# Performance work log

Hardware: AMD Instinct MI355X
Metric: run time of the kernel (lower is better)

Reference implementation:

```python
import jax, jax.numpy as jnp
import numpy as np

DIM = 768
HEADS = 12
HD = DIM // HEADS
B, NX, NY = 8, 1024, 1024
GRID = 32
FREQ = 100.0
MLP_HID = 4 * DIM
EPS = 1e-5


def _grid_pos(batch, n, grid):
    g = int(np.sqrt(n))
    yy, xx = jnp.meshgrid(jnp.arange(g, dtype=jnp.int32), jnp.arange(g, dtype=jnp.int32), indexing='ij')
    pos = jnp.stack([yy.reshape(-1), xx.reshape(-1)], axis=-1)  # [N,2]
    return jnp.broadcast_to(pos[None], (batch, n, 2))


def setup_inputs() -> dict:
    key = jax.random.key(0)
    ks = jax.random.split(key, 16)
    s = 0.02
    inp = {
        'x': jax.random.normal(ks[0], (B, NX, DIM), jnp.float32),
        'y': jax.random.normal(ks[1], (B, NY, DIM), jnp.float32),
        'xpos': _grid_pos(B, NX, GRID),
        'ypos': _grid_pos(B, NY, GRID),
        # norms (gamma, beta)
        'norm1_g': jnp.ones((DIM,), jnp.float32), 'norm1_b': jnp.zeros((DIM,), jnp.float32),
        'norm2_g': jnp.ones((DIM,), jnp.float32), 'norm2_b': jnp.zeros((DIM,), jnp.float32),
        'norm3_g': jnp.ones((DIM,), jnp.float32), 'norm3_b': jnp.zeros((DIM,), jnp.float32),
        'normy_g': jnp.ones((DIM,), jnp.float32), 'normy_b': jnp.zeros((DIM,), jnp.float32),
        # self-attn: fused qkv (no bias, qkv_bias=False), out proj (with bias)
        'qkv_w': jax.random.normal(ks[2], (DIM, 3 * DIM), jnp.float32) * s,
        'attn_proj_w': jax.random.normal(ks[3], (DIM, DIM), jnp.float32) * s,
        'attn_proj_b': jnp.zeros((DIM,), jnp.float32),
        # cross-attn: separate q/k/v (no bias), out proj (with bias)
        'projq_w': jax.random.normal(ks[4], (DIM, DIM), jnp.float32) * s,
        'projk_w': jax.random.normal(ks[5], (DIM, DIM), jnp.float32) * s,
        'projv_w': jax.random.normal(ks[6], (DIM, DIM), jnp.float32) * s,
        'cross_proj_w': jax.random.normal(ks[7], (DIM, DIM), jnp.float32) * s,
        'cross_proj_b': jnp.zeros((DIM,), jnp.float32),
        # MLP
        'fc1_w': jax.random.normal(ks[8], (DIM, MLP_HID), jnp.float32) * s,
        'fc1_b': jnp.zeros((MLP_HID,), jnp.float32),
        'fc2_w': jax.random.normal(ks[9], (MLP_HID, DIM), jnp.float32) * s,
        'fc2_b': jnp.zeros((DIM,), jnp.float32),
    }
    return inp


def layernorm(x, g, b):
    m = jnp.mean(x, axis=-1, keepdims=True)
    v = jnp.mean(jnp.square(x - m), axis=-1, keepdims=True)
    return (x - m) * jax.lax.rsqrt(v + EPS) * g + b


def rope1d(tok, pos):
    # tok: [B,H,N,D], pos: [B,N] int
    D = tok.shape[-1]
    inv = 1.0 / (FREQ ** (jnp.arange(0, D, 2, dtype=jnp.float32) / D))  # [D/2]
    f = pos[:, None, :, None].astype(jnp.float32) * inv  # [B,1,N,D/2]
    emb = jnp.concatenate([f, f], axis=-1)  # [B,1,N,D]
    cos, sin = jnp.cos(emb), jnp.sin(emb)
    t1, t2 = jnp.split(tok, 2, axis=-1)
    rot = jnp.concatenate([-t2, t1], axis=-1)
    return tok * cos + rot * sin


def rope2d(tok, pos):
    # first half of head dim rotated by y-coord, second half by x-coord
    ty, tx = jnp.split(tok, 2, axis=-1)
    return jnp.concatenate([rope1d(ty, pos[..., 0]), rope1d(tx, pos[..., 1])], axis=-1)


def sdpa(q, k, v):
    scale = q.shape[-1] ** -0.5
    a = jax.nn.softmax(jnp.einsum('bhqd,bhkd->bhqk', q, k) * scale, axis=-1)
    return jnp.einsum('bhqk,bhkd->bhqd', a, v)


def split_heads(t):  # [B,N,C] -> [B,H,N,HD]
    Bv, N, C = t.shape
    return t.reshape(Bv, N, HEADS, HD).transpose(0, 2, 1, 3)


def merge_heads(t):  # [B,H,N,HD] -> [B,N,C]
    Bv, H, N, D = t.shape
    return t.transpose(0, 2, 1, 3).reshape(Bv, N, H * D)


def reference(x, y, xpos, ypos,
              norm1_g, norm1_b, norm2_g, norm2_b, norm3_g, norm3_b, normy_g, normy_b,
              qkv_w, attn_proj_w, attn_proj_b,
              projq_w, projk_w, projv_w, cross_proj_w, cross_proj_b,
              fc1_w, fc1_b, fc2_w, fc2_b):
    # --- self attention ---
    h = layernorm(x, norm1_g, norm1_b)
    qkv = h @ qkv_w  # [B,N,3C]
    q, k, v = (split_heads(t) for t in jnp.split(qkv, 3, axis=-1))
    q = rope2d(q, xpos)
    k = rope2d(k, xpos)
    x = x + merge_heads(sdpa(q, k, v)) @ attn_proj_w + attn_proj_b

    # --- cross attention ---
    y_ = layernorm(y, normy_g, normy_b)
    hq = layernorm(x, norm2_g, norm2_b)
    q = rope2d(split_heads(hq @ projq_w), xpos)
    k = rope2d(split_heads(y_ @ projk_w), ypos)
    v = split_heads(y_ @ projv_w)
    x = x + merge_heads(sdpa(q, k, v)) @ cross_proj_w + cross_proj_b

    # --- MLP ---
    h = layernorm(x, norm3_g, norm3_b)
    x = x + jax.nn.gelu(h @ fc1_w + fc1_b, approximate=False) @ fc2_w + fc2_b
    return (x, y)
```

## Files before the change

kernel.cpp:

```cpp
#include <hip/hip_runtime.h>
#include <hip/hip_bf16.h>
#include <math.h>

#define DIM 768
#define HEADS 12
#define HD 64
#define BB 8
#define NN 1024
#define EPSV 1e-5f

typedef unsigned int uint32;
typedef unsigned short ushort_t;
using short8 = __attribute__((ext_vector_type(8))) short;
using f32x4 = __attribute__((ext_vector_type(4))) float;

static __device__ inline ushort_t f2b(float v) {
    uint32 u = __float_as_uint(v);
    return (ushort_t)((u + 0x7FFFu + ((u >> 16) & 1u)) >> 16);
}
static __device__ inline float b2f(ushort_t v) {
    return __uint_as_float((uint32)v << 16);
}

static __device__ inline float erf_fast(float x) {
    float ax = fabsf(x);
    float t = __frcp_rn(1.0f + 0.3275911f * ax);
    float p = t * (0.254829592f + t * (-0.284496736f + t * (1.421413741f +
              t * (-1.453152027f + t * 1.061405429f))));
    float e = 1.0f - p * __expf(-ax * ax);
    return copysignf(e, x);
}

static __device__ __forceinline__ void gload_lds16(const ushort_t* g, ushort_t* l) {
    __builtin_amdgcn_global_load_lds(
        (const __attribute__((address_space(1))) void*)g,
        (__attribute__((address_space(3))) void*)l, 16, 0, 0);
}

__global__ __launch_bounds__(256) void ln_bf16(const float* __restrict__ in,
                                               const float* __restrict__ g,
                                               const float* __restrict__ b,
                                               ushort_t* __restrict__ out) {
    int r = blockIdx.x;
    const float* x = in + (size_t)r * DIM;
    ushort_t* o = out + (size_t)r * DIM;
    int t = threadIdx.x;
    float v0 = x[t], v1 = x[t + 256], v2 = x[t + 512];
    float s = v0 + v1 + v2;
    float s2 = v0 * v0 + v1 * v1 + v2 * v2;
    for (int off = 32; off; off >>= 1) {
        s += __shfl_xor(s, off);
        s2 += __shfl_xor(s2, off);
    }
    __shared__ float ls[4], lq[4];
    int wid = t >> 6;
    if ((t & 63) == 0) { ls[wid] = s; lq[wid] = s2; }
    __syncthreads();
    s = ls[0] + ls[1] + ls[2] + ls[3];
    s2 = lq[0] + lq[1] + lq[2] + lq[3];
    float mean = s * (1.0f / DIM);
    float var = s2 * (1.0f / DIM) - mean * mean;
    float rs = rsqrtf(var + EPSV);
    o[t]       = f2b((v0 - mean) * rs * g[t]       + b[t]);
    o[t + 256] = f2b((v1 - mean) * rs * g[t + 256] + b[t + 256]);
    o[t + 512] = f2b((v2 - mean) * rs * g[t + 512] + b[t + 512]);
}

struct XArgs {
    const float* src[8];
    ushort_t* dst[8];
    int K[8], N[8];
    int tstart[9];
};
__global__ __launch_bounds__(256) void xform_w(XArgs a) {
    __shared__ float tl[32][33];
    int t = blockIdx.x;
    int w = 0;
    while (t >= a.tstart[w + 1]) w++;
    int lt = t - a.tstart[w];
    int ntn = a.N[w] >> 5;
    int k0 = (lt / ntn) * 32, n0 = (lt % ntn) * 32;
    const float* src = a.src[w];
    ushort_t* dst = a.dst[w];
    int K = a.K[w], N = a.N[w];
    int rr = threadIdx.x >> 5, cc = threadIdx.x & 31;
#pragma unroll
    for (int u = 0; u < 4; u++)
        tl[rr + u * 8][cc] = src[(size_t)(k0 + rr + u * 8) * N + n0 + cc];
    __syncthreads();
#pragma unroll
    for (int u = 0; u < 4; u++)
        dst[(size_t)(n0 + rr + u * 8) * K + k0 + cc] = f2b(tl[cc][rr + u * 8]);
}

template <int ACT, int OBF16>
__global__ __launch_bounds__(256) void gemm_mfma(const ushort_t* __restrict__ A,
                                                 const ushort_t* __restrict__ Wt,
                                                 const float* __restrict__ bias,
                                                 const float* res,
                                                 void* Cout, int M, int N, int K) {
    __shared__ ushort_t lds[4][128 * 32];
    int bid = blockIdx.x;
    int xcd = bid & 7, rr = bid >> 3;
    int bx = rr >> 3;
    int by = xcd * 8 + (rr & 7);
    int m0 = by * 128, n0 = bx * 128;
    int tid = threadIdx.x;
    int wid = tid >> 6, lane = tid & 63;
    int wm = wid >> 1, wn = wid & 1;
    int l15 = lane & 15, lh = lane >> 4;

    int srow = lane >> 2, cslot = lane & 3;

    auto STAGE = [&](int buf, int k0) {
#pragma unroll
        for (int inst = 0; inst < 2; inst++) {
            int r0 = (wid * 2 + inst) * 16 + srow;
            int swzr = (r0 & 3) ^ ((r0 >> 2) & 3);
            int csrc = (cslot ^ swzr) << 3;
            gload_lds16(A + (size_t)(m0 + r0) * K + k0 + csrc,
                        &lds[buf * 2 + 0][(wid * 2 + inst) * 512]);
            gload_lds16(Wt + (size_t)(n0 + r0) * K + k0 + csrc,
                        &lds[buf * 2 + 1][(wid * 2 + inst) * 512]);
        }
    };

    STAGE(0, 0);
    f32x4 acc[4][4] = {};
    __syncthreads();

    int nT = K >> 5;
    int cur = 0;
    for (int t = 0; t < nT; t++) {
        if (t + 1 < nT) STAGE(cur ^ 1, (t + 1) << 5);
        short8 af[4], bfr[4];
#pragma unroll
        for (int i = 0; i < 4; i++) {
            int rA = wm * 64 + i * 16 + l15;
            int sA = lh ^ ((rA & 3) ^ ((rA >> 2) & 3));
            af[i] = *(const short8*)&lds[cur * 2 + 0][rA * 32 + (sA << 3)];
            int rB = wn * 64 + i * 16 + l15;
            int sB = lh ^ ((rB & 3) ^ ((rB >> 2) & 3));
            bfr[i] = *(const short8*)&lds[cur * 2 + 1][rB * 32 + (sB << 3)];
        }
#pragma unroll
        for (int i = 0; i < 4; i++)
#pragma unroll
            for (int j = 0; j < 4; j++)
                acc[i][j] = __builtin_amdgcn_mfma_f32_16x16x32_bf16(
                    af[i], bfr[j], acc[i][j], 0, 0, 0);
        __syncthreads();
        cur ^= 1;
    }

    float* ep = (float*)&lds[0][0] + wid * 1088;
    int erow = lane >> 2, ecol = (lane & 3) * 16;
#pragma unroll
    for (int i = 0; i < 4; i++) {
#pragma unroll
        for (int j = 0; j < 4; j++) {
            int n = n0 + wn * 64 + j * 16 + l15;
            float bv = bias ? bias[n] : 0.0f;
#pragma unroll
            for (int r = 0; r < 4; r++) {
                float v = acc[i][j][r] + bv;
                if (ACT == 1) v = 0.5f * v * (1.0f + erf_fast(v * 0.70710678118654752f));
                ep[(lh * 4 + r) * 68 + j * 16 + l15] = v;
            }
        }
        int m = m0 + wm * 64 + i * 16 + erow;
        size_t off = (size_t)m * N + n0 + wn * 64 + ecol;
        float vv[16];
#pragma unroll
        for (int u = 0; u < 4; u++)
            *(float4*)&vv[u * 4] = *(float4*)&ep[erow * 68 + ecol + u * 4];
        if (res) {
#pragma unroll
            for (int u = 0; u < 4; u++) {
                float4 rv = *(const float4*)(res + off + u * 4);
                vv[u * 4 + 0] += rv.x;
                vv[u * 4 + 1] += rv.y;
                vv[u * 4 + 2] += rv.z;
                vv[u * 4 + 3] += rv.w;
            }
        }
        if (OBF16) {
            ushort_t tb[16];
#pragma unroll
            for (int u = 0; u < 16; u++) tb[u] = f2b(vv[u]);
            *(uint4*)((ushort_t*)Cout + off)     = *(uint4*)&tb[0];
            *(uint4*)((ushort_t*)Cout + off + 8) = *(uint4*)&tb[8];
        } else {
#pragma unroll
            for (int u = 0; u < 4; u++)
                *(float4*)((float*)Cout + off + u * 4) = *(float4*)&vv[u * 4];
        }
    }
}

__global__ __launch_bounds__(256) void rope2_bf16(ushort_t* __restrict__ ta,
                                                  const int* __restrict__ pa, int sa,
                                                  ushort_t* __restrict__ tb,
                                                  const int* __restrict__ pb, int sb,
                                                  int rt) {
    int idx = blockIdx.x * 256 + threadIdx.x;
    ushort_t* t;
    const int* pos;
    int rowStride;
    if (idx >= rt) { idx -= rt; t = tb; pos = pb; rowStride = sb; }
    else           { t = ta; pos = pa; rowStride = sa; }
    int i = idx & 15;
    int half = (idx >> 4) & 1;
    int h = (idx >> 5) % HEADS;
    int bn = idx / (HEADS * 32);
    int p = pos[(size_t)bn * 2 + half];
    float inv = powf(100.0f, -(float)i / 16.0f);
    float f = (float)p * inv;
    float c, s;
    sincosf(f, &s, &c);
    ushort_t* base = t + (size_t)bn * rowStride + h * HD + half * 32;
    float t1 = b2f(base[i]), t2 = b2f(base[i + 16]);
    base[i]      = f2b(t1 * c - t2 * s);
    base[i + 16] = f2b(t2 * c + t1 * s);
}

__global__ __launch_bounds__(256) void transpose_v(const ushort_t* __restrict__ src,
                                                   int ss, ushort_t* __restrict__ dst) {
    __shared__ ushort_t tl[64][66];
    int bid = blockIdx.x;
    int nt = bid & 15;
    int h = (bid >> 4) % HEADS;
    int b = bid / (16 * HEADS);
    int n0 = nt * 64;
    int t = threadIdx.x;
    int r = t >> 2, c0 = (t & 3) * 16;
    const ushort_t* s = src + ((size_t)(b * NN) + n0 + r) * ss + h * HD + c0;
    *(uint4*)&tl[r][c0]     = *(const uint4*)s;
    *(uint4*)&tl[r][c0 + 8] = *(const uint4*)(s + 8);
    __syncthreads();
    ushort_t* d = dst + (((size_t)(b * HEADS + h)) * HD + r) * NN + n0 + c0;
    ushort_t tmp[16];
#pragma unroll
    for (int u = 0; u < 16; u++) tmp[u] = tl[c0 + u][r];
    *(uint4*)d       = *(uint4*)tmp;
    *(uint4*)(d + 8) = *(uint4*)(tmp + 8);
}

__global__ __launch_bounds__(256) void attn_mfma(const ushort_t* __restrict__ Q, int sq,
                                                 const ushort_t* __restrict__ K, int sk,
                                                 const ushort_t* __restrict__ VT,
                                                 ushort_t* __restrict__ O, int so) {
    __shared__ ushort_t Qs[64][72];
    __shared__ ushort_t Ks[64][72];
    __shared__ ushort_t Vs[64][72];
    __shared__ ushort_t Ps[64][72];

    int g = blockIdx.x;
    int bid = (g & 7) * 192 + (g >> 3);
    int qb = bid & 15;
    int h = (bid >> 4) % HEADS;
    int b = bid / (16 * HEADS);
    int n0 = qb * 64;

    int tid = threadIdx.x;
    int lane = tid & 63, wq = tid >> 6;
    int l15 = lane & 15, lh = lane >> 4;

    const ushort_t* Qbase = Q + (size_t)b * NN * sq + h * HD;
    const ushort_t* Kbase = K + (size_t)b * NN * sk + h * HD;
    const ushort_t* VTbase = VT + ((size_t)(b * HEADS + h)) * HD * NN;
    ushort_t* Obase = O + (size_t)b * NN * so + h * HD;

    int row = tid >> 2, c0 = (tid & 3) * 16;
    {
        const ushort_t* src = Qbase + (size_t)(n0 + row) * sq + c0;
        uint4 q0 = *(const uint4*)src;
        uint4 q1 = *(const uint4*)(src + 8);
        ushort_t* qp0 = (ushort_t*)&q0;
        ushort_t* qp1 = (ushort_t*)&q1;
        ushort_t t0[8], t1[8];
#pragma unroll
        for (int u = 0; u < 8; u++) {
            t0[u] = f2b(b2f(qp0[u]) * 0.125f);
            t1[u] = f2b(b2f(qp1[u]) * 0.125f);
        }
        *(uint4*)&Qs[row][c0]     = *(uint4*)t0;
        *(uint4*)&Qs[row][c0 + 8] = *(uint4*)t1;
    }

    const ushort_t* kp = Kbase + (size_t)row * sk + c0;
    const ushort_t* vp = VTbase + (size_t)row * NN + c0;
    uint4 rk0 = *(const uint4*)kp, rk1 = *(const uint4*)(kp + 8);
    uint4 rv0 = *(const uint4*)vp, rv1 = *(const uint4*)(vp + 8);

    short8 ones;
#pragma unroll
    for (int u = 0; u < 8; u++) ones[u] = (short)0x3F80;

    f32x4 oacc[4] = {};
    f32x4 oaccS = {};
    float mrow[4] = {-1e30f, -1e30f, -1e30f, -1e30f};

    for (int kt = 0; kt < NN / 64; kt++) {
        __syncthreads();
        *(uint4*)&Ks[row][c0]     = rk0;
        *(uint4*)&Ks[row][c0 + 8] = rk1;
        *(uint4*)&Vs[row][c0]     = rv0;
        *(uint4*)&Vs[row][c0 + 8] = rv1;
        __syncthreads();
        if (kt + 1 < NN / 64) {
            const ushort_t* kp2 = kp + (size_t)(kt + 1) * 64 * sk;
            const ushort_t* vp2 = vp + (size_t)(kt + 1) * 64;
            rk0 = *(const uint4*)kp2;
            rk1 = *(const uint4*)(kp2 + 8);
            rv0 = *(const uint4*)vp2;
            rv1 = *(const uint4*)(vp2 + 8);
        }

        f32x4 s[4] = {};
#pragma unroll
        for (int ks8 = 0; ks8 < 2; ks8++) {
            short8 aq = *(const short8*)&Qs[wq * 16 + l15][ks8 * 32 + lh * 8];
#pragma unroll
            for (int j = 0; j < 4; j++) {
                short8 bk = *(const short8*)&Ks[j * 16 + l15][ks8 * 32 + lh * 8];
                s[j] = __builtin_amdgcn_mfma_f32_16x16x32_bf16(aq, bk, s[j], 0, 0, 0);
            }
        }

        float corr[4];
#pragma unroll
        for (int r = 0; r < 4; r++) {
            float v0 = s[0][r], v1 = s[1][r], v2 = s[2][r], v3 = s[3][r];
            float rm = fmaxf(fmaxf(v0, v1), fmaxf(v2, v3));
            rm = fmaxf(rm, __shfl_xor(rm, 1));
            rm = fmaxf(rm, __shfl_xor(rm, 2));
            rm = fmaxf(rm, __shfl_xor(rm, 4));
            rm = fmaxf(rm, __shfl_xor(rm, 8));
            float mn = fmaxf(mrow[r], rm);
            corr[r] = __expf(mrow[r] - mn);
            mrow[r] = mn;
            float p0 = __expf(v0 - mn), p1 = __expf(v1 - mn);
            float p2 = __expf(v2 - mn), p3 = __expf(v3 - mn);
            int qrow = wq * 16 + lh * 4 + r;
            Ps[qrow][0 * 16 + l15] = f2b(p0);
            Ps[qrow][1 * 16 + l15] = f2b(p1);
            Ps[qrow][2 * 16 + l15] = f2b(p2);
            Ps[qrow][3 * 16 + l15] = f2b(p3);
        }
#pragma unroll
        for (int r = 0; r < 4; r++) {
            oaccS[r] *= corr[r];
#pragma unroll
            for (int j = 0; j < 4; j++) oacc[j][r] *= corr[r];
        }

#pragma unroll
        for (int ks8 = 0; ks8 < 2; ks8++) {
            short8 ap = *(const short8*)&Ps[wq * 16 + l15][ks8 * 32 + lh * 8];
#pragma unroll
            for (int j = 0; j < 4; j++) {
                short8 bv = *(const short8*)&Vs[j * 16 + l15][ks8 * 32 + lh * 8];
                oacc[j] = __builtin_amdgcn_mfma_f32_16x16x32_bf16(ap, bv, oacc[j], 0, 0, 0);
            }
            oaccS = __builtin_amdgcn_mfma_f32_16x16x32_bf16(ap, ones, oaccS, 0, 0, 0);
        }
    }

#pragma unroll
    for (int r = 0; r < 4; r++) {
        float inv = 1.0f / oaccS[r];
        int prow = wq * 16 + lh * 4 + r;
#pragma unroll
        for (int j = 0; j < 4; j++)
            Ps[prow][j * 16 + l15] = f2b(oacc[j][r] * inv);
    }
    int erow = lane >> 2, ecol = (lane & 3) * 16;
    uint4 w0 = *(uint4*)&Ps[wq * 16 + erow][ecol];
    uint4 w1 = *(uint4*)&Ps[wq * 16 + erow][ecol + 8];
    ushort_t* op = Obase + (size_t)(n0 + wq * 16 + erow) * so + ecol;
    *(uint4*)op       = w0;
    *(uint4*)(op + 8) = w1;
}

__global__ __launch_bounds__(256) void fill_f32(float* __restrict__ out, float v, int n) {
    int i = blockIdx.x * 256 + threadIdx.x;
    if (i < n) out[i] = v;
}

extern "C" void kernel_launch(void* const* d_in, const int* in_sizes, int n_in,
                              void* d_out, int out_size, void* d_ws, size_t ws_size,
                              hipStream_t stream) {
    const float* x = (const float*)d_in[0];
    const float* y = (const float*)d_in[1];
    const int* xpos = (const int*)d_in[2];
    const int* ypos = (const int*)d_in[3];
    const float* norm1_g = (const float*)d_in[4];
    const float* norm1_b = (const float*)d_in[5];
    const float* norm2_g = (const float*)d_in[6];
    const float* norm2_b = (const float*)d_in[7];
    const float* norm3_g = (const float*)d_in[8];
    const float* norm3_b = (const float*)d_in[9];
    const float* normy_g = (const float*)d_in[10];
    const float* normy_b = (const float*)d_in[11];
    const float* qkv_w = (const float*)d_in[12];
    const float* attn_proj_w = (const float*)d_in[13];
    const float* attn_proj_b = (const float*)d_in[14];
    const float* projq_w = (const float*)d_in[15];
    const float* projk_w = (const float*)d_in[16];
    const float* projv_w = (const float*)d_in[17];
    const float* cross_proj_w = (const float*)d_in[18];
    const float* cross_proj_b = (const float*)d_in[19];
    const float* fc1_w = (const float*)d_in[20];
    const float* fc1_b = (const float*)d_in[21];
    const float* fc2_w = (const float*)d_in[22];
    const float* fc2_b = (const float*)d_in[23];
    float* out = (float*)d_out;

    const size_t SZ = (size_t)BB * NN * DIM;
    const int ROWS = BB * NN;

    const size_t WS_NEED = SZ * 4 + SZ * 2 + 4 * SZ * 2 + 9437184ull * 2;

    {
        const int expect[24] = {
            (int)SZ, (int)SZ, BB * NN * 2, BB * NN * 2,
            DIM, DIM, DIM, DIM, DIM, DIM, DIM, DIM,
            DIM * 3 * DIM, DIM * DIM, DIM,
            DIM * DIM, DIM * DIM, DIM * DIM, DIM * DIM, DIM,
            DIM * 4 * DIM, 4 * DIM, 4 * DIM * DIM, DIM};
        float sentinel = 0.0f;
        if (n_in != 24) sentinel = 2000.0f;
        else {
            for (int i = 0; i < 24; i++)
                if (in_sizes[i] != expect[i]) { sentinel = 1000.0f + i; break; }
        }
        if (sentinel == 0.0f && ws_size < WS_NEED) sentinel = 3000.0f;
        if (sentinel == 0.0f && out_size != (int)(2 * SZ)) sentinel = 4000.0f;
        if (sentinel != 0.0f) {
            fill_f32<<<(int)((SZ + 255) / 256), 256, 0, stream>>>(out, sentinel, (int)SZ);
            return;
        }
    }

    float* bufX = (float*)d_ws;
    ushort_t* bufAb = (ushort_t*)(bufX + SZ);
    ushort_t* bufQKVb = bufAb + SZ;
    ushort_t* wts = bufQKVb + 4 * SZ;

    ushort_t* qkvT = wts;
    ushort_t* apT  = qkvT + 2304 * 768;
    ushort_t* pqT  = apT + 768 * 768;
    ushort_t* pkT  = pqT + 768 * 768;
    ushort_t* pvT  = pkT + 768 * 768;
    ushort_t* cpT  = pvT + 768 * 768;
    ushort_t* fc1T = cpT + 768 * 768;
    ushort_t* fc2T = fc1T + 3072 * 768;
    ushort_t* HID  = bufQKVb;

    XArgs xa;
    xa.src[0] = qkv_w;        xa.dst[0] = qkvT; xa.K[0] = 768;  xa.N[0] = 2304;
    xa.src[1] = attn_proj_w;  xa.dst[1] = apT;  xa.K[1] = 768;  xa.N[1] = 768;
    xa.src[2] = projq_w;      xa.dst[2] = pqT;  xa.K[2] = 768;  xa.N[2] = 768;
    xa.src[3] = projk_w;      xa.dst[3] = pkT;  xa.K[3] = 768;  xa.N[3] = 768;
    xa.src[4] = projv_w;      xa.dst[4] = pvT;  xa.K[4] = 768;  xa.N[4] = 768;
    xa.src[5] = cross_proj_w; xa.dst[5] = cpT;  xa.K[5] = 768;  xa.N[5] = 768;
    xa.src[6] = fc1_w;        xa.dst[6] = fc1T; xa.K[6] = 768;  xa.N[6] = 3072;
    xa.src[7] = fc2_w;        xa.dst[7] = fc2T; xa.K[7] = 3072; xa.N[7] = 768;
    int acc_t = 0;
    for (int i = 0; i < 8; i++) {
        xa.tstart[i] = acc_t;
        acc_t += (xa.K[i] / 32) * (xa.N[i] / 32);
    }
    xa.tstart[8] = acc_t;
    xform_w<<<acc_t, 256, 0, stream>>>(xa);

    const int rt = ROWS * HEADS * 32;
    const int attnGrid = BB * HEADS * (NN / 64);
    ushort_t* VTg;

    ln_bf16<<<ROWS, 256, 0, stream>>>(x, norm1_g, norm1_b, bufAb);
    gemm_mfma<0, 1><<<64 * 18, 256, 0, stream>>>(bufAb, qkvT, nullptr, nullptr,
                                                 bufQKVb, ROWS, 2304, 768);
    rope2_bf16<<<2 * rt / 256, 256, 0, stream>>>(bufQKVb, xpos, 2304,
                                                 bufQKVb + DIM, xpos, 2304, rt);
    VTg = bufQKVb + 3 * SZ;
    transpose_v<<<attnGrid, 256, 0, stream>>>(bufQKVb + 2 * DIM, 2304, VTg);
    attn_mfma<<<attnGrid, 256, 0, stream>>>(bufQKVb, 2304, bufQKVb + DIM, 2304,
                                            VTg, bufAb, DIM);
    gemm_mfma<0, 0><<<64 * 6, 256, 0, stream>>>(bufAb, apT, attn_proj_b, x,
                                                bufX, ROWS, 768, 768);

    ushort_t* Qc = bufQKVb;
    ushort_t* KVc = bufQKVb + SZ;
    ln_bf16<<<ROWS, 256, 0, stream>>>(bufX, norm2_g, norm2_b, bufAb);
    gemm_mfma<0, 1><<<64 * 6, 256, 0, stream>>>(bufAb, pqT, nullptr, nullptr,
                                                Qc, ROWS, 768, 768);
    ln_bf16<<<ROWS, 256, 0, stream>>>(y, normy_g, normy_b, bufAb);
    gemm_mfma<0, 1><<<64 * 12, 256, 0, stream>>>(bufAb, pkT, nullptr, nullptr,
                                                 KVc, ROWS, 1536, 768);
    rope2_bf16<<<2 * rt / 256, 256, 0, stream>>>(Qc, xpos, 768,
                                                 KVc, ypos, 1536, rt);
    VTg = bufQKVb + 3 * SZ;
    transpose_v<<<attnGrid, 256, 0, stream>>>(KVc + DIM, 1536, VTg);
    attn_mfma<<<attnGrid, 256, 0, stream>>>(Qc, 768, KVc, 1536, VTg, bufAb, DIM);
    gemm_mfma<0, 0><<<64 * 6, 256, 0, stream>>>(bufAb, cpT, cross_proj_b, bufX,
                                                bufX, ROWS, 768, 768);

    ln_bf16<<<ROWS, 256, 0, stream>>>(bufX, norm3_g, norm3_b, bufAb);
    gemm_mfma<1, 1><<<64 * 24, 256, 0, stream>>>(bufAb, fc1T, fc1_b, nullptr,
                                                 HID, ROWS, 3072, 768);
    gemm_mfma<0, 0><<<64 * 6, 256, 0, stream>>>(HID, fc2T, fc2_b, bufX,
                                                out, ROWS, 768, 3072);

    hipMemcpyAsync(out + SZ, y, SZ * sizeof(float), hipMemcpyDeviceToDevice, stream);
}
```

Measured before the change: 532.7 us.

## Double-buffer K/V tiles in LDS with XOR swizzle and one barrier per step

```diff
diff --git a/kernel.cpp b/kernel.cpp
--- a/kernel.cpp
+++ b/kernel.cpp
@@ -251,8 +251,8 @@
                                                  const ushort_t* __restrict__ VT,
                                                  ushort_t* __restrict__ O, int so) {
     __shared__ ushort_t Qs[64][72];
-    __shared__ ushort_t Ks[64][72];
-    __shared__ ushort_t Vs[64][72];
+    __shared__ ushort_t Kb[2][64 * 64];
+    __shared__ ushort_t Vb[2][64 * 64];
     __shared__ ushort_t Ps[64][72];
 
     int g = blockIdx.x;
@@ -265,13 +265,18 @@
     int tid = threadIdx.x;
     int lane = tid & 63, wq = tid >> 6;
     int l15 = lane & 15, lh = lane >> 4;
+    int xr = l15 & 7;
 
     const ushort_t* Qbase = Q + (size_t)b * NN * sq + h * HD;
     const ushort_t* Kbase = K + (size_t)b * NN * sk + h * HD;
     const ushort_t* VTbase = VT + ((size_t)(b * HEADS + h)) * HD * NN;
     ushort_t* Obase = O + (size_t)b * NN * so + h * HD;
 
-    int row = tid >> 2, c0 = (tid & 3) * 16;
+    int row = tid >> 2, ch = (tid & 3) * 2;
+    int c0 = ch << 3;
+    int wo0 = row * 64 + ((ch ^ (row & 7)) << 3);
+    int wo1 = row * 64 + (((ch + 1) ^ (row & 7)) << 3);
+
     {
         const ushort_t* src = Qbase + (size_t)(n0 + row) * sq + c0;
         uint4 q0 = *(const uint4*)src;
@@ -290,8 +295,21 @@
 
     const ushort_t* kp = Kbase + (size_t)row * sk + c0;
     const ushort_t* vp = VTbase + (size_t)row * NN + c0;
+
     uint4 rk0 = *(const uint4*)kp, rk1 = *(const uint4*)(kp + 8);
     uint4 rv0 = *(const uint4*)vp, rv1 = *(const uint4*)(vp + 8);
+    *(uint4*)&Kb[0][wo0] = rk0;
+    *(uint4*)&Kb[0][wo1] = rk1;
+    *(uint4*)&Vb[0][wo0] = rv0;
+    *(uint4*)&Vb[0][wo1] = rv1;
+    {
+        const ushort_t* kp2 = kp + (size_t)64 * sk;
+        const ushort_t* vp2 = vp + 64;
+        rk0 = *(const uint4*)kp2;
+        rk1 = *(const uint4*)(kp2 + 8);
+        rv0 = *(const uint4*)vp2;
+        rv1 = *(const uint4*)(vp2 + 8);
+    }
 
     short8 ones;
 #pragma unroll
@@ -301,16 +319,19 @@
     f32x4 oaccS = {};
     float mrow[4] = {-1e30f, -1e30f, -1e30f, -1e30f};
 
+    __syncthreads();
+
     for (int kt = 0; kt < NN / 64; kt++) {
-        __syncthreads();
-        *(uint4*)&Ks[row][c0]     = rk0;
-        *(uint4*)&Ks[row][c0 + 8] = rk1;
-        *(uint4*)&Vs[row][c0]     = rv0;
-        *(uint4*)&Vs[row][c0 + 8] = rv1;
-        __syncthreads();
+        int cb = kt & 1;
         if (kt + 1 < NN / 64) {
-            const ushort_t* kp2 = kp + (size_t)(kt + 1) * 64 * sk;
-            const ushort_t* vp2 = vp + (size_t)(kt + 1) * 64;
+            *(uint4*)&Kb[cb ^ 1][wo0] = rk0;
+            *(uint4*)&Kb[cb ^ 1][wo1] = rk1;
+            *(uint4*)&Vb[cb ^ 1][wo0] = rv0;
+            *(uint4*)&Vb[cb ^ 1][wo1] = rv1;
+        }
+        if (kt + 2 < NN / 64) {
+            const ushort_t* kp2 = kp + (size_t)(kt + 2) * 64 * sk;
+            const ushort_t* vp2 = vp + (size_t)(kt + 2) * 64;
             rk0 = *(const uint4*)kp2;
             rk1 = *(const uint4*)(kp2 + 8);
             rv0 = *(const uint4*)vp2;
@@ -323,7 +344,8 @@
             short8 aq = *(const short8*)&Qs[wq * 16 + l15][ks8 * 32 + lh * 8];
 #pragma unroll
             for (int j = 0; j < 4; j++) {
-                short8 bk = *(const short8*)&Ks[j * 16 + l15][ks8 * 32 + lh * 8];
+                int cc = (ks8 * 4 + lh) ^ xr;
+                short8 bk = *(const short8*)&Kb[cb][(j * 16 + l15) * 64 + (cc << 3)];
                 s[j] = __builtin_amdgcn_mfma_f32_16x16x32_bf16(aq, bk, s[j], 0, 0, 0);
             }
         }
@@ -360,11 +382,13 @@
             short8 ap = *(const short8*)&Ps[wq * 16 + l15][ks8 * 32 + lh * 8];
 #pragma unroll
             for (int j = 0; j < 4; j++) {
-                short8 bv = *(const short8*)&Vs[j * 16 + l15][ks8 * 32 + lh * 8];
+                int cc = (ks8 * 4 + lh) ^ xr;
+                short8 bv = *(const short8*)&Vb[cb][(j * 16 + l15) * 64 + (cc << 3)];
                 oacc[j] = __builtin_amdgcn_mfma_f32_16x16x32_bf16(ap, bv, oacc[j], 0, 0, 0);
             }
             oaccS = __builtin_amdgcn_mfma_f32_16x16x32_bf16(ap, ones, oaccS, 0, 0, 0);
         }
+        __syncthreads();
     }
 
 #pragma unroll
```

New measurement: 525.2 us. About the same (-1.4%).
